# Kernel optimization log

Hardware: AMD Instinct MI355X
Metric: run time of the kernel (lower is better)

Reference implementation:

```python
import jax, jax.numpy as jnp
import numpy as np
from jax import lax

B, N = 16, 4096
S1, S2, K = 512, 256, 32
EPS = 1e-5


def setup_inputs() -> dict:
    key = jax.random.key(0)
    ks = jax.random.split(key, 8)
    p = lambda k, shape: jax.random.normal(k, shape, jnp.float32) * 0.05
    return {
        "x": jax.random.normal(ks[0], (B, 3, N), jnp.float32),
        "w1": p(ks[1], (64, 3)),
        "w2": p(ks[2], (64, 64)),
        "g1": jnp.ones(64, jnp.float32), "b1": jnp.zeros(64, jnp.float32),
        "g2": jnp.ones(64, jnp.float32), "b2": jnp.zeros(64, jnp.float32),
        "sg1_w1": p(ks[3], (128, 128)), "sg1_w2": p(ks[4], (128, 128)),
        "sg1_g1": jnp.ones(128, jnp.float32), "sg1_b1": jnp.zeros(128, jnp.float32),
        "sg1_g2": jnp.ones(128, jnp.float32), "sg1_b2": jnp.zeros(128, jnp.float32),
        "sg2_w1": p(ks[5], (256, 256)), "sg2_w2": p(ks[6], (256, 256)),
        "sg2_g1": jnp.ones(256, jnp.float32), "sg2_b1": jnp.zeros(256, jnp.float32),
        "sg2_g2": jnp.ones(256, jnp.float32), "sg2_b2": jnp.zeros(256, jnp.float32),
    }


def fps(coords, s):
    # furthest point sampling, starts at index 0 (as pointnet2 CUDA kernel)
    Bc, Nc, _ = coords.shape
    def step(carry, _):
        dist, far = carry
        centroid = jnp.take_along_axis(coords, far[:, None, None], axis=1)  # [B,1,3]
        d = jnp.sum((coords - centroid) ** 2, -1)                            # [B,N]
        dist = jnp.minimum(dist, d)
        return (dist, jnp.argmax(dist, -1)), far
    init = (jnp.full((Bc, Nc), 1e10, coords.dtype), jnp.zeros((Bc,), jnp.int32))
    _, idxs = lax.scan(step, init, None, length=s)
    return idxs.T  # [B,s]


def gather(pts, idx):
    # pts [B,N,C], idx [B,...] -> [B,...,C]
    return jax.vmap(lambda p, i: p[i])(pts, idx)


def sqdist(a, b):
    # [B,S,3],[B,N,3] -> [B,S,N]
    return (jnp.sum(a ** 2, -1)[..., None] + jnp.sum(b ** 2, -1)[:, None, :]
            - 2.0 * jnp.einsum('bsc,bnc->bsn', a, b))


def bn_relu_grouped(y, g, b):
    # y [B,s,k,O]; BatchNorm1d over (B*s, O, k) => stats over (0,1,2)
    m = y.mean((0, 1, 2), keepdims=True)
    v = y.var((0, 1, 2), keepdims=True)
    return jax.nn.relu((y - m) / jnp.sqrt(v + EPS) * g + b)


def sg_block(f_bnc, coords, s, w1, g1, b1, w2, g2, b2):
    # f_bnc [B,N,C]; coords [B,N,3]
    fidx = fps(coords, s)                      # [B,s]
    new_xyz = gather(coords, fidx)             # [B,s,3]
    new_feat = gather(f_bnc, fidx)             # [B,s,C]
    d = sqdist(new_xyz, coords)                # [B,s,N]
    _, knn_idx = lax.top_k(-d, K)              # [B,s,K]
    grouped = gather(f_bnc, knn_idx)           # [B,s,K,C]
    center = new_feat[:, :, None]              # [B,s,1,C]
    agg = jnp.concatenate([grouped - center,
                           jnp.broadcast_to(center, grouped.shape)], -1)  # [B,s,K,2C]
    y = bn_relu_grouped(jnp.einsum('bskd,od->bsko', agg, w1), g1, b1)
    y = bn_relu_grouped(jnp.einsum('bskd,od->bsko', y, w2), g2, b2)
    return new_xyz, y.max(2)                   # [B,s,O]


def point_cbr(f, w, g, b):
    # f [B,C,N]; conv1d k=1 + BN (stats over (0,2)) + relu
    y = jnp.einsum('bcn,oc->bon', f, w)
    m = y.mean((0, 2), keepdims=True)
    v = y.var((0, 2), keepdims=True)
    return jax.nn.relu((y - m) / jnp.sqrt(v + EPS) * g[None, :, None] + b[None, :, None])


def reference(x, w1, w2, g1, b1, g2, b2,
              sg1_w1, sg1_w2, sg1_g1, sg1_b1, sg1_g2, sg1_b2,
              sg2_w1, sg2_w2, sg2_g1, sg2_b1, sg2_g2, sg2_b2):
    xyz = x.transpose(0, 2, 1)                                  # [B,N,3]
    f = point_cbr(point_cbr(x, w1, g1, b1), w2, g2, b2)         # [B,64,N]
    xyz1, f1 = sg_block(f.transpose(0, 2, 1), xyz, S1,
                        sg1_w1, sg1_g1, sg1_b1, sg1_w2, sg1_g2, sg1_b2)  # f1 [B,S1,128]
    _, f2 = sg_block(f1, xyz1, S2,
                     sg2_w1, sg2_g1, sg2_b1, sg2_w2, sg2_g2, sg2_b2)     # [B,S2,256]
    return f2.transpose(0, 2, 1)                                # [B,256,S2]
```

## Files before the change

### kernel.cpp

```cpp
#include <hip/hip_runtime.h>

#define EPSF 1e-5f
#define NBINS 16
#define STATS_REGION 8192

using short8  = __attribute__((ext_vector_type(8))) short;
using float4v = __attribute__((ext_vector_type(4))) float;

__device__ __forceinline__ unsigned short f2bf(float f){
    unsigned u = __float_as_uint(f);
    unsigned r = u + 0x7FFFu + ((u >> 16) & 1u);
    return (unsigned short)(r >> 16);
}
__device__ __forceinline__ float bf2f(unsigned short h){
    return __uint_as_float(((unsigned)h) << 16);
}
__device__ __forceinline__ unsigned monou(float f){
    unsigned u = __float_as_uint(f);
    return u ^ (((unsigned)((int)u >> 31)) | 0x80000000u);
}

template<int CTRL, int RMASK>
__device__ __forceinline__ float fmax_dpp(float x){
    int xi = __float_as_int(x);
    int yi = __builtin_amdgcn_update_dpp(xi, xi, CTRL, RMASK, 0xf, false);
    return fmaxf(x, __int_as_float(yi));
}
__device__ __forceinline__ float wave_max_dpp(float x){
    x = fmax_dpp<0x111, 0xf>(x);
    x = fmax_dpp<0x112, 0xf>(x);
    x = fmax_dpp<0x114, 0xf>(x);
    x = fmax_dpp<0x118, 0xf>(x);
    x = fmax_dpp<0x142, 0xa>(x);
    x = fmax_dpp<0x143, 0xc>(x);
    return __int_as_float(__builtin_amdgcn_readlane(__float_as_int(x), 63));
}

__device__ __forceinline__ void compute_ss(const float* __restrict__ st,
                                           const float* __restrict__ g,
                                           const float* __restrict__ bb,
                                           float* lss, int C, float invCnt,
                                           int t, int TPB){
    for (int c = t; c < C; c += TPB){
        float s = 0.f, q = 0.f;
        #pragma unroll 4
        for (int bin = 0; bin < NBINS; bin++){
            s += st[bin * 2 * C + c];
            q += st[bin * 2 * C + C + c];
        }
        float m = s * invCnt;
        float v = q * invCnt - m * m;
        float sc = g[c] / sqrtf(v + EPSF);
        lss[c] = sc;
        lss[C + c] = bb[c] - m * sc;
    }
}

template<int NP, int SO, int AW, bool STRIDED>
__device__ void fps_body(char* smem, const float* __restrict__ coords,
                         int* __restrict__ fidx, float* __restrict__ xyz_out, int b){
    float* lx = (float*)smem;
    float* ly = lx + NP;
    float* lz = ly + NP;
    unsigned long long* red = (unsigned long long*)(lz + NP);
    const int t = threadIdx.x;
    const float* cb = coords + (size_t)b * 3 * NP;
    constexpr int PS = NP / 256;
    #pragma unroll
    for (int i = 0; i < PS; i++){
        int n = i * 256 + t;
        float X, Y, Z;
        if (STRIDED){ X = cb[n]; Y = cb[NP + n]; Z = cb[2*NP + n]; }
        else        { X = cb[n*3]; Y = cb[n*3+1]; Z = cb[n*3+2]; }
        lx[n] = X; ly[n] = Y; lz[n] = Z;
    }
    __syncthreads();
    if (AW == 1 && t >= 64) return;
    constexpr int TPB = AW * 64;
    constexpr int P = NP / TPB;
    float px[P], py[P], pz[P], dist[P];
    #pragma unroll
    for (int i = 0; i < P; i++){
        int n = t * P + i;
        px[i] = lx[n]; py[i] = ly[n]; pz[i] = lz[n];
        dist[i] = 1e10f;
    }
    int cur = 0;
    for (int it = 0; it < SO; ++it){
        if (t == 0){
            fidx[b * SO + it] = cur;
            float* xo = xyz_out + ((size_t)b * SO + it) * 3;
            xo[0] = lx[cur]; xo[1] = ly[cur]; xo[2] = lz[cur];
        }
        float cx = lx[cur], cy = ly[cur], cz = lz[cur];
        float bd = -1.f;
        int bn = 0;
        {
            #pragma clang fp contract(off)
            #pragma unroll
            for (int i = 0; i < P; i++){
                float dx = px[i] - cx, dy = py[i] - cy, dz = pz[i] - cz;
                float d = (dx*dx + dy*dy) + dz*dz;
                float nd = fminf(dist[i], d);
                dist[i] = nd;
                if (nd > bd){ bd = nd; bn = t * P + i; }
            }
        }
        float wm = wave_max_dpp(bd);
        unsigned long long msk = __ballot(bd == wm);
        int wl = (int)(__ffsll(msk) - 1);
        int n_w = __builtin_amdgcn_readlane(bn, wl);
        if constexpr (AW == 1){
            cur = n_w;
        } else {
            int par = it & 1;
            if ((t & 63) == 0){
                red[par * AW + (t >> 6)] = ((unsigned long long)__float_as_uint(wm) << 32)
                                         | (unsigned)(0xFFFFFFFFu - (unsigned)n_w);
            }
            __syncthreads();
            unsigned long long best = red[par * AW];
            #pragma unroll
            for (int j = 1; j < AW; j++){
                unsigned long long v = red[par * AW + j];
                best = best > v ? best : v;
            }
            cur = (int)(0xFFFFFFFFu - (unsigned)(best & 0xFFFFFFFFull));
        }
    }
}

template<int NC, int SO, bool STRIDED>
__device__ void knn_body(const float* __restrict__ coords,
                         const float* __restrict__ samp,
                         int* __restrict__ knno, int row){
    const int b = row / SO, s = row % SO;
    const int lane = threadIdx.x & 63;
    const float* cb = coords + (size_t)b * 3 * NC;
    const float* a = samp + ((size_t)b * SO + s) * 3;
    float ax = a[0], ay = a[1], az = a[2];
    float asq = ax*ax + ay*ay + az*az;
    constexpr int J = NC / 64;
    unsigned long long t8[8];
    #pragma unroll
    for (int i = 0; i < 8; i++) t8[i] = ~0ULL;
    for (int j = 0; j < J; j++){
        int n = j * 64 + lane;
        float bx, by, bz;
        if (STRIDED){ bx = cb[n]; by = cb[NC + n]; bz = cb[2*NC + n]; }
        else        { bx = cb[n*3]; by = cb[n*3+1]; bz = cb[n*3+2]; }
        float bsq = bx*bx + by*by + bz*bz;
        float dot = ax*bx + ay*by + az*bz;
        float d = (asq + bsq) - 2.0f * dot;
        unsigned long long key = ((unsigned long long)monou(d) << 32) | (unsigned)n;
        if (key < t8[7]){
            t8[7] = key;
            #pragma unroll
            for (int i = 6; i >= 0; i--){
                if (t8[i] > t8[i+1]){ unsigned long long tm = t8[i]; t8[i] = t8[i+1]; t8[i+1] = tm; }
            }
        }
    }
    unsigned long long cur = t8[0];
    int myout = 0;
    bool bad = false;
    int popped = 0;
    for (int r = 0; r < 32; r++){
        unsigned long long m = cur;
        #pragma unroll
        for (int o2 = 32; o2 > 0; o2 >>= 1){
            unsigned long long v = __shfl_xor(m, o2, 64);
            m = m < v ? m : v;
        }
        if (lane == r) myout = (int)(unsigned)(m & 0xFFFFFFFFull);
        if (cur == m){
            #pragma unroll
            for (int i = 0; i < 7; i++) t8[i] = t8[i+1];
            t8[7] = ~0ULL;
            cur = t8[0];
            popped++;
            if (J > 8 && popped == 8 && r < 31) bad = true;
        }
    }
    if (__any(bad)){
        unsigned long long last = 0;
        for (int r = 0; r < 32; r++){
            unsigned long long mk = ~0ULL;
            for (int j = 0; j < J; j++){
                int n = j * 64 + lane;
                float bx, by, bz;
                if (STRIDED){ bx = cb[n]; by = cb[NC + n]; bz = cb[2*NC + n]; }
                else        { bx = cb[n*3]; by = cb[n*3+1]; bz = cb[n*3+2]; }
                float bsq = bx*bx + by*by + bz*bz;
                float dot = ax*bx + ay*by + az*bz;
                float d = (asq + bsq) - 2.0f * dot;
                unsigned long long key = ((unsigned long long)monou(d) << 32) | (unsigned)n;
                if (key > last && key < mk) mk = key;
            }
            unsigned long long m = mk;
            #pragma unroll
            for (int o2 = 32; o2 > 0; o2 >>= 1){
                unsigned long long v = __shfl_xor(m, o2, 64);
                m = m < v ? m : v;
            }
            if (lane == r) myout = (int)(unsigned)(m & 0xFFFFFFFFull);
            last = m;
        }
    }
    if (lane < 32) knno[((size_t)b * SO + s) * 32 + lane] = myout;
}

__device__ void pc_body(char* smem, const float* __restrict__ x,
                        const float* __restrict__ w1, const float* __restrict__ w2,
                        const float* __restrict__ g1, const float* __restrict__ b1,
                        const float* __restrict__ xmom, float* __restrict__ y2t,
                        float* __restrict__ stY2, int blk){
    float* w1s  = (float*)smem;
    float* wt   = w1s + 192;
    float* lss1 = wt + 4096;
    float* hS   = lss1 + 128;
    int t = threadIdx.x;
    if (t < 192) w1s[t] = w1[t];
    for (int i = t; i < 4096; i += 256){ int o = i & 63, c = i >> 6; wt[c*64+o] = w2[o*64+c]; }
    __syncthreads();
    if (t < 64){
        float mu0 = xmom[0] * (1.f/65536.f), mu1 = xmom[1] * (1.f/65536.f), mu2 = xmom[2] * (1.f/65536.f);
        float M00 = xmom[3] * (1.f/65536.f), M01 = xmom[4] * (1.f/65536.f), M02 = xmom[5] * (1.f/65536.f);
        float M11 = xmom[6] * (1.f/65536.f), M12 = xmom[7] * (1.f/65536.f), M22 = xmom[8] * (1.f/65536.f);
        float a = w1s[t*3], b = w1s[t*3+1], c = w1s[t*3+2];
        float mo = a*mu0 + b*mu1 + c*mu2;
        float e2 = a*a*M00 + b*b*M11 + c*c*M22 + 2.f*(a*b*M01 + a*c*M02 + b*c*M12);
        float var = e2 - mo*mo;
        float sc = g1[t] / sqrtf(var + EPSF);
        lss1[t] = sc;
        lss1[64 + t] = b1[t] - mo * sc;
    }
    __syncthreads();
    int p = t & 63, cg = t >> 6;
    int point = blk * 64 + p;
    int b = point >> 12, n = point & 4095;
    const float* xb = x + (size_t)b * 12288;
    float x0 = xb[n], x1 = xb[4096 + n], x2 = xb[8192 + n];
    #pragma unroll
    for (int i = 0; i < 16; i++){
        int c = cg * 16 + i;
        float y1 = x0 * w1s[c*3] + x1 * w1s[c*3+1] + x2 * w1s[c*3+2];
        hS[p * 65 + c] = fmaxf(y1 * lss1[c] + lss1[64 + c], 0.f);
    }
    __syncthreads();
    float4v acc[4];
    #pragma unroll
    for (int i = 0; i < 4; i++) acc[i] = (float4v){0.f,0.f,0.f,0.f};
    for (int c = 0; c < 64; c++){
        float hv = hS[p * 65 + c];
        #pragma unroll
        for (int i = 0; i < 4; i++){
            float4v w4 = *(const float4v*)&wt[c*64 + cg*16 + i*4];
            acc[i] += hv * w4;
        }
    }
    float* dst = y2t + (size_t)point * 64 + cg * 16;
    #pragma unroll
    for (int i = 0; i < 4; i++) *(float4v*)(dst + i*4) = acc[i];
    float s16[16], q16[16];
    #pragma unroll
    for (int i = 0; i < 16; i++){
        float v = acc[i >> 2][i & 3];
        s16[i] = v; q16[i] = v * v;
    }
    #pragma unroll
    for (int i = 0; i < 16; i++){
        #pragma unroll
        for (int o = 32; o > 0; o >>= 1){
            s16[i] += __shfl_xor(s16[i], o, 64);
            q16[i] += __shfl_xor(q16[i], o, 64);
        }
    }
    if (p == 0){
        float* sdst = stY2 + (size_t)(blk & (NBINS - 1)) * 128;
        #pragma unroll
        for (int i = 0; i < 16; i++){
            atomicAdd(&sdst[cg * 16 + i], s16[i]);
            atomicAdd(&sdst[64 + cg * 16 + i], q16[i]);
        }
    }
}


template<int O, int D>
__device__ __forceinline__ void pack_body(const float* __restrict__ w,
                                          unsigned short* __restrict__ pk, int tid){
    constexpr int CH = D / 32;
    constexpr int TOT = (O/16) * CH * 64;
    if (tid >= TOT) return;
    int lane = tid & 63;
    int fc = tid >> 6;
    int ch = fc % CH;
    int ot = fc / CH;
    int o  = ot * 16 + (lane & 15);
    int kb = ch * 32 + (lane >> 4) * 8;
    #pragma unroll
    for (int j = 0; j < 8; j++) pk[(size_t)tid * 8 + j] = f2bf(w[(size_t)o * D + kb + j]);
}

template<int D, int O>
__device__ __forceinline__ void mfma_store_y(const short* A, const short* wp,
                                             unsigned short* Y, float* lsum, float* lsq,
                                             int blk, int t){
    constexpr int RS = D + 8;
    constexpr int CH = D / 32;
    constexpr int OPW = (O / 16) / 4;
    int lane = t & 63, wv = t >> 6;
    int col = lane & 15, quad = lane >> 4;
    for (int oi = 0; oi < OPW; ++oi){
        int ot = wv * OPW + oi;
        for (int mt = 0; mt < 4; ++mt){
            float4v acc = {0.f, 0.f, 0.f, 0.f};
            #pragma unroll
            for (int ch = 0; ch < CH; ++ch){
                short8 a  = *(const short8*)(A + (mt*16 + col) * RS + ch*32 + quad*8);
                short8 bf = *(const short8*)(wp + ((size_t)(ot*CH + ch) * 64 + lane) * 8);
                acc = __builtin_amdgcn_mfma_f32_16x16x32_bf16(a, bf, acc, 0, 0, 0);
            }
            float s4 = 0.f, q4 = 0.f;
            size_t rowbase = (size_t)blk * 64 + mt * 16 + quad * 4;
            #pragma unroll
            for (int r = 0; r < 4; r++){
                float v = acc[r];
                s4 += v; q4 += v * v;
                Y[(rowbase + r) * O + ot * 16 + col] = f2bf(v);
            }
            s4 += __shfl_xor(s4, 16, 64); s4 += __shfl_xor(s4, 32, 64);
            q4 += __shfl_xor(q4, 16, 64); q4 += __shfl_xor(q4, 32, 64);
            if (quad == 0){ lsum[ot*16 + col] += s4; lsq[ot*16 + col] += q4; }
        }
    }
}

template<int D, int O>
__device__ __forceinline__ void mfma_maxmin(const short* A, const short* wp,
                                            float2* mxmn, float* lsum, float* lsq,
                                            int blk, int t){
    constexpr int RS = D + 8;
    constexpr int CH = D / 32;
    constexpr int OPW = (O / 16) / 4;
    int lane = t & 63, wv = t >> 6;
    int col = lane & 15, quad = lane >> 4;
    for (int oi = 0; oi < OPW; ++oi){
        int ot = wv * OPW + oi;
        float mx[2] = {-1e30f, -1e30f}, mn[2] = {1e30f, 1e30f};
        for (int mt = 0; mt < 4; ++mt){
            float4v acc = {0.f, 0.f, 0.f, 0.f};
            #pragma unroll
            for (int ch = 0; ch < CH; ++ch){
                short8 a  = *(const short8*)(A + (mt*16 + col) * RS + ch*32 + quad*8);
                short8 bf = *(const short8*)(wp + ((size_t)(ot*CH + ch) * 64 + lane) * 8);
                acc = __builtin_amdgcn_mfma_f32_16x16x32_bf16(a, bf, acc, 0, 0, 0);
            }
            int g = mt >> 1;
            float s4 = 0.f, q4 = 0.f;
            #pragma unroll
            for (int r = 0; r < 4; r++){
                float v = acc[r];
                s4 += v; q4 += v * v;
                mx[g] = fmaxf(mx[g], v);
                mn[g] = fminf(mn[g], v);
            }
            s4 += __shfl_xor(s4, 16, 64); s4 += __shfl_xor(s4, 32, 64);
            q4 += __shfl_xor(q4, 16, 64); q4 += __shfl_xor(q4, 32, 64);
            if (quad == 0){ lsum[ot*16 + col] += s4; lsq[ot*16 + col] += q4; }
        }
        #pragma unroll
        for (int g = 0; g < 2; g++){
            mx[g] = fmaxf(mx[g], __shfl_xor(mx[g], 16, 64));
            mx[g] = fmaxf(mx[g], __shfl_xor(mx[g], 32, 64));
            mn[g] = fminf(mn[g], __shfl_xor(mn[g], 16, 64));
            mn[g] = fminf(mn[g], __shfl_xor(mn[g], 32, 64));
            if (quad == 0){
                mxmn[((size_t)(blk * 2 + g)) * O + ot * 16 + col] = make_float2(mx[g], mn[g]);
            }
        }
    }
}

template<int DH, int O, int S, int NPTS, int MODE>
__device__ void gemm1_body(char* smem, const void* __restrict__ fsrc,
                           const float* __restrict__ fst, const float* __restrict__ fg,
                           const float* __restrict__ fb, float finv,
                           const int* __restrict__ fidx, const int* __restrict__ knn,
                           const short* __restrict__ wp, unsigned short* __restrict__ Y,
                           float* __restrict__ sums, int blk){
    constexpr int D = 2 * DH;
    constexpr int RS = D + 8;
    short* A    = (short*)smem;
    float* lsum = (float*)(smem + 64*RS*2);
    float* lsq  = lsum + O;
    float* lssf = lsq + O;
    int t = threadIdx.x;
    for (int i = t; i < O; i += 256){ lsum[i] = 0.f; lsq[i] = 0.f; }
    compute_ss(fst, fg, fb, lssf, DH, finv, t, 256);
    __syncthreads();
    for (int g = 0; g < 2; ++g){
        int gid = blk * 2 + g;
        int b = gid / S;
        int cidx = fidx[gid];
        int kk = t >> 3;
        int p  = t & 7;
        int nb = knn[(size_t)gid * 32 + kk];
        constexpr int E = D / 8;
        int d0 = p * E;
        short* row = A + (g * 32 + kk) * RS;
        if (MODE == 1){
            const float* fcp = (const float*)fsrc + ((size_t)b * NPTS + cidx) * DH;
            const float* fnp = (const float*)fsrc + ((size_t)b * NPTS + nb) * DH;
            #pragma unroll
            for (int e = 0; e < E; e++){
                int d = d0 + e;
                float v;
                if (d < DH){
                    float a = fmaxf(fnp[d] * lssf[d] + lssf[DH + d], 0.f);
                    float c = fmaxf(fcp[d] * lssf[d] + lssf[DH + d], 0.f);
                    v = a - c;
                } else {
                    v = fmaxf(fcp[d - DH] * lssf[d - DH] + lssf[DH + d - DH], 0.f);
                }
                row[d] = (short)f2bf(v);
            }
        } else {
            const float2* fcp = (const float2*)fsrc + ((size_t)b * NPTS + cidx) * DH;
            const float2* fnp = (const float2*)fsrc + ((size_t)b * NPTS + nb) * DH;
            #pragma unroll
            for (int e = 0; e < E; e++){
                int d = d0 + e;
                float v;
                if (d < DH){
                    float sc = lssf[d], sh = lssf[DH + d];
                    float2 a2 = fnp[d], c2 = fcp[d];
                    float av = fmaxf((sc > 0.f ? a2.x : a2.y) * sc + sh, 0.f);
                    float cv = fmaxf((sc > 0.f ? c2.x : c2.y) * sc + sh, 0.f);
                    v = av - cv;
                } else {
                    int dd = d - DH;
                    float sc = lssf[dd], sh = lssf[DH + dd];
                    float2 c2 = fcp[dd];
                    v = fmaxf((sc > 0.f ? c2.x : c2.y) * sc + sh, 0.f);
                }
                row[d] = (short)f2bf(v);
            }
        }
    }
    __syncthreads();
    mfma_store_y<D, O>(A, wp, Y, lsum, lsq, blk, t);
    __syncthreads();
    float* dst = sums + (size_t)(blk & (NBINS - 1)) * 2 * O;
    for (int i = t; i < O; i += 256){
        atomicAdd(&dst[i], lsum[i]);
        atomicAdd(&dst[O + i], lsq[i]);
    }
}

template<int D, int O>
__device__ void gemm2m_body(char* smem, const unsigned short* __restrict__ Yin,
                            const float* __restrict__ st, const float* __restrict__ g,
                            const float* __restrict__ bb, float inv,
                            const short* __restrict__ wp, float2* __restrict__ mxmn,
                            float* __restrict__ sums, int blk){
    constexpr int RS = D + 8;
    short* A    = (short*)smem;
    float* lsum = (float*)(smem + 64*RS*2);
    float* lsq  = lsum + O;
    float* lss  = lsq + O;
    int t = threadIdx.x;
    for (int i = t; i < O; i += 256){ lsum[i] = 0.f; lsq[i] = 0.f; }
    compute_ss(st, g, bb, lss, D, inv, t, 256);
    __syncthreads();
    {
        int row = t >> 2;
        int d0 = (t & 3) * (D / 4);
        const unsigned short* src = Yin + ((size_t)blk * 64 + row) * D + d0;
        short* dst = A + row * RS + d0;
        #pragma unroll
        for (int e = 0; e < D/4; e++){
            float v = bf2f(src[e]);
            int d = d0 + e;
            v = fmaxf(v * lss[d] + lss[D + d], 0.f);
            dst[e] = (short)f2bf(v);
        }
    }
    __syncthreads();
    mfma_maxmin<D, O>(A, wp, mxmn, lsum, lsq, blk, t);
    __syncthreads();
    float* dst = sums + (size_t)(blk & (NBINS - 1)) * 2 * O;
    for (int i = t; i < O; i += 256){
        atomicAdd(&dst[i], lsum[i]);
        atomicAdd(&dst[O + i], lsq[i]);
    }
}


__global__ __launch_bounds__(256) void k1_statsx_pack(const float* __restrict__ x,
                                                      float* __restrict__ xmom,
                                                      const float* w1, const float* w2,
                                                      const float* w3, const float* w4,
                                                      unsigned short* p1, unsigned short* p2,
                                                      unsigned short* p3, unsigned short* p4){
    int blk = blockIdx.x, t = threadIdx.x;
    if (blk == 0){
        float a[9] = {0,0,0,0,0,0,0,0,0};
        for (int gid = t; gid < 65536; gid += 256){
            int b = gid >> 12, n = gid & 4095;
            const float* xb = x + (size_t)b * 12288;
            float x0 = xb[n], x1 = xb[4096 + n], x2 = xb[8192 + n];
            a[0] += x0; a[1] += x1; a[2] += x2;
            a[3] += x0*x0; a[4] += x0*x1; a[5] += x0*x2;
            a[6] += x1*x1; a[7] += x1*x2; a[8] += x2*x2;
        }
        __shared__ float red[4][9];
        #pragma unroll
        for (int k = 0; k < 9; k++){
            float v = a[k];
            for (int o = 32; o > 0; o >>= 1) v += __shfl_down(v, o, 64);
            a[k] = v;
        }
        if ((t & 63) == 0){
            #pragma unroll
            for (int k = 0; k < 9; k++) red[t >> 6][k] = a[k];
        }
        __syncthreads();
        if (t == 0){
            #pragma unroll
            for (int k = 0; k < 9; k++)
                xmom[k] = red[0][k] + red[1][k] + red[2][k] + red[3][k];
        }
    } else {
        int pb = blk - 1;
        if (pb < 8)       pack_body<128,128>(w1, p1, pb * 256 + t);
        else if (pb < 16) pack_body<128,128>(w2, p2, (pb - 8) * 256 + t);
        else if (pb < 48) pack_body<256,256>(w3, p3, (pb - 16) * 256 + t);
        else              pack_body<256,256>(w4, p4, (pb - 48) * 256 + t);
    }
}

__global__ __launch_bounds__(256) void k2_fps1_pc(const float* __restrict__ x,
                                                  int* __restrict__ fidx1, float* __restrict__ xyz1,
                                                  const float* w1, const float* w2,
                                                  const float* g1, const float* b1,
                                                  const float* __restrict__ xmom,
                                                  float* __restrict__ y2t,
                                                  float* __restrict__ stY2){
    extern __shared__ char smem[];
    if (blockIdx.x < 16) fps_body<4096,512,4,true>(smem, x, fidx1, xyz1, blockIdx.x);
    else                 pc_body(smem, x, w1, w2, g1, b1, xmom, y2t, stY2, blockIdx.x - 16);
}

__global__ __launch_bounds__(256) void k3_knn1(const float* __restrict__ x,
                                               const float* __restrict__ xyz1,
                                               int* __restrict__ knn1){
    int row = blockIdx.x * 4 + (threadIdx.x >> 6);
    knn_body<4096,512,true>(x, xyz1, knn1, row);
}

__global__ __launch_bounds__(256) void k4_fps2_gemm1a(const float* __restrict__ xyz1,
                                                      int* __restrict__ fidx2, float* __restrict__ xyz2,
                                                      const float* __restrict__ y2t,
                                                      const float* __restrict__ stY2,
                                                      const float* g2, const float* b2,
                                                      const int* __restrict__ fidx1,
                                                      const int* __restrict__ knn1,
                                                      const short* __restrict__ wp1,
                                                      unsigned short* __restrict__ Y1,
                                                      float* __restrict__ stG1a){
    extern __shared__ char smem[];
    if (blockIdx.x < 16)
        fps_body<512,256,1,false>(smem, xyz1, fidx2, xyz2, blockIdx.x);
    else
        gemm1_body<64,128,512,4096,1>(smem, y2t, stY2, g2, b2, 1.f/65536.f,
                                      fidx1, knn1, wp1, Y1, stG1a, blockIdx.x - 16);
}

__global__ __launch_bounds__(256) void k5_knn2_gemm2ma(const float* __restrict__ xyz1,
                                                       const float* __restrict__ xyz2,
                                                       int* __restrict__ knn2,
                                                       const unsigned short* __restrict__ Y1,
                                                       const float* __restrict__ stG1a,
                                                       const float* s1g1, const float* s1b1,
                                                       const short* __restrict__ wp2,
                                                       float2* __restrict__ mxmn1,
                                                       float* __restrict__ stG2a){
    extern __shared__ char smem[];
    if (blockIdx.x < 1024){
        int row = blockIdx.x * 4 + (threadIdx.x >> 6);
        knn_body<512,256,false>(xyz1, xyz2, knn2, row);
    } else {
        gemm2m_body<128,128>(smem, Y1, stG1a, s1g1, s1b1, 1.f/262144.f,
                             wp2, mxmn1, stG2a, blockIdx.x - 1024);
    }
}

template<int DH, int O, int S, int NPTS, int MODE>
__global__ __launch_bounds__(256) void gemm1_kernel(const void* fsrc, const float* fst,
                                                    const float* fg, const float* fb, float finv,
                                                    const int* fidx, const int* knn,
                                                    const short* wp, unsigned short* Y,
                                                    float* sums){
    extern __shared__ char smem[];
    gemm1_body<DH,O,S,NPTS,MODE>(smem, fsrc, fst, fg, fb, finv, fidx, knn, wp, Y, sums, blockIdx.x);
}

template<int D, int O>
__global__ __launch_bounds__(256) void gemm2m_kernel(const unsigned short* Yin, const float* st,
                                                     const float* g, const float* bb, float inv,
                                                     const short* wp, float2* mxmn, float* sums){
    extern __shared__ char smem[];
    gemm2m_body<D,O>(smem, Yin, st, g, bb, inv, wp, mxmn, sums, blockIdx.x);
}

__global__ __launch_bounds__(256) void final_out_kernel(const float2* __restrict__ mxmn,
                                                        const float* __restrict__ st,
                                                        const float* __restrict__ g,
                                                        const float* __restrict__ bb,
                                                        float inv,
                                                        float* __restrict__ out){
    __shared__ float lss[512];
    __shared__ float tile[64][65];
    int t = threadIdx.x;
    compute_ss(st, g, bb, lss, 256, inv, t, 256);
    __syncthreads();
    int blk = blockIdx.x;
    int b = blk >> 4;
    int ot = (blk >> 2) & 3, stt = blk & 3;
    int o_in = t & 63, sg = t >> 6;
    int o = ot * 64 + o_in;
    float sc = lss[o], sh = lss[256 + o];
    for (int si = 0; si < 16; si++){
        int s = stt * 64 + sg * 16 + si;
        int row = b * 256 + s;
        float2 v2 = mxmn[(size_t)row * 256 + o];
        float v = (sc > 0.f ? v2.x : v2.y) * sc + sh;
        tile[sg * 16 + si][o_in] = fmaxf(v, 0.f);
    }
    __syncthreads();
    int s_in = t & 63, og = t >> 6;
    for (int oj = 0; oj < 16; oj++){
        int oo = ot * 64 + og * 16 + oj;
        out[(size_t)b * 65536 + (size_t)oo * 256 + stt * 64 + s_in] = tile[s_in][og * 16 + oj];
    }
}

extern "C" void kernel_launch(void* const* d_in, const int* in_sizes, int n_in,
                              void* d_out, int out_size, void* d_ws, size_t ws_size,
                              hipStream_t stream) {
    const float* x    = (const float*)d_in[0];
    const float* w1   = (const float*)d_in[1];
    const float* w2   = (const float*)d_in[2];
    const float* g1   = (const float*)d_in[3];
    const float* b1   = (const float*)d_in[4];
    const float* g2   = (const float*)d_in[5];
    const float* b2   = (const float*)d_in[6];
    const float* s1w1 = (const float*)d_in[7];
    const float* s1w2 = (const float*)d_in[8];
    const float* s1g1 = (const float*)d_in[9];
    const float* s1b1 = (const float*)d_in[10];
    const float* s1g2 = (const float*)d_in[11];
    const float* s1b2 = (const float*)d_in[12];
    const float* s2w1 = (const float*)d_in[13];
    const float* s2w2 = (const float*)d_in[14];
    const float* s2g1 = (const float*)d_in[15];
    const float* s2b1 = (const float*)d_in[16];
    const float* s2g2 = (const float*)d_in[17];
    const float* s2b2 = (const float*)d_in[18];
    float* out = (float*)d_out;

    char* ws = (char*)d_ws;
    size_t off = 0;
    auto take = [&](size_t bytes){ size_t r = off; off += (bytes + 255) & ~(size_t)255; return r; };
    float* y2t     = (float*)(ws + take(16u*4096u*64u*4u));
    float2* mxmn1  = (float2*)(ws + take(8192u*128u*8u));
    float2* mxmn2  = (float2*)(ws + take(4096u*256u*8u));
    int*   fidx1   = (int*)  (ws + take(16u*512u*4u));
    float* xyz1    = (float*)(ws + take(16u*512u*3u*4u));
    int*   fidx2   = (int*)  (ws + take(16u*256u*4u));
    float* xyz2    = (float*)(ws + take(16u*256u*3u*4u));
    int*   knn1    = (int*)  (ws + take(16u*512u*32u*4u));
    int*   knn2    = (int*)  (ws + take(16u*256u*32u*4u));
    unsigned short* wp1 = (unsigned short*)(ws + take(128u*128u*2u));
    unsigned short* wp2 = (unsigned short*)(ws + take(128u*128u*2u));
    unsigned short* wp3 = (unsigned short*)(ws + take(256u*256u*2u));
    unsigned short* wp4 = (unsigned short*)(ws + take(256u*256u*2u));
    float* stats   = (float*)(ws + take(6u*STATS_REGION*4u));
    char*  regA    = ws + take(67108864u);
    (void)in_sizes; (void)n_in; (void)out_size; (void)ws_size;

    float* xmom    = stats + 0*STATS_REGION;
    float* stY2    = stats + 1*STATS_REGION;
    float* stG1a   = stats + 2*STATS_REGION;
    float* stG2a   = stats + 3*STATS_REGION;
    float* stG1b   = stats + 4*STATS_REGION;
    float* stG2b   = stats + 5*STATS_REGION;

    unsigned short* Y1 = (unsigned short*)regA;

    hipMemsetAsync(stats, 0, 6u*STATS_REGION*4u, stream);

    k1_statsx_pack<<<81, 256, 0, stream>>>(x, xmom, s1w1, s1w2, s2w1, s2w2, wp1, wp2, wp3, wp4);
    k2_fps1_pc<<<1040, 256, 49216, stream>>>(x, fidx1, xyz1, w1, w2, g1, b1, xmom, y2t, stY2);
    k3_knn1<<<2048, 256, 0, stream>>>(x, xyz1, knn1);
    k4_fps2_gemm1a<<<4112, 256, 18944, stream>>>(xyz1, fidx2, xyz2, y2t, stY2, g2, b2,
                                                 fidx1, knn1, (const short*)wp1, Y1, stG1a);
    k5_knn2_gemm2ma<<<5120, 256, 19456, stream>>>(xyz1, xyz2, knn2, Y1, stG1a, s1g1, s1b1,
                                                  (const short*)wp2, mxmn1, stG2a);
    gemm1_kernel<128,256,256,512,2><<<2048, 256, 36864, stream>>>(
        mxmn1, stG2a, s1g2, s1b2, 1.f/262144.f, fidx2, knn2, (const short*)wp3, Y1, stG1b);
    gemm2m_kernel<256,256><<<2048, 256, 37888, stream>>>(
        Y1, stG1b, s2g1, s2b1, 1.f/131072.f, (const short*)wp4, mxmn2, stG2b);
    final_out_kernel<<<256, 256, 0, stream>>>(mxmn2, stG2b, s2g2, s2b2, 1.f/131072.f, out);
}
```

Measured before the change: 939.9 us.

## Vectorize LDS row stores, raise FPS priority, parallelize input moment stats

Measured after the change: 884.8 us. 5.9% less time.

```diff
diff --git a/kernel.cpp b/kernel.cpp
--- a/kernel.cpp
+++ b/kernel.cpp
@@ -59,6 +59,7 @@
 template<int NP, int SO, int AW, bool STRIDED>
 __device__ void fps_body(char* smem, const float* __restrict__ coords,
                          int* __restrict__ fidx, float* __restrict__ xyz_out, int b){
+    asm volatile("s_setprio 3");
     float* lx = (float*)smem;
     float* ly = lx + NP;
     float* lz = ly + NP;
@@ -414,38 +415,48 @@
             const float* fcp = (const float*)fsrc + ((size_t)b * NPTS + cidx) * DH;
             const float* fnp = (const float*)fsrc + ((size_t)b * NPTS + nb) * DH;
             #pragma unroll
-            for (int e = 0; e < E; e++){
-                int d = d0 + e;
-                float v;
-                if (d < DH){
-                    float a = fmaxf(fnp[d] * lssf[d] + lssf[DH + d], 0.f);
-                    float c = fmaxf(fcp[d] * lssf[d] + lssf[DH + d], 0.f);
-                    v = a - c;
-                } else {
-                    v = fmaxf(fcp[d - DH] * lssf[d - DH] + lssf[DH + d - DH], 0.f);
+            for (int e8 = 0; e8 < E; e8 += 8){
+                short8 pk;
+                #pragma unroll
+                for (int e = 0; e < 8; e++){
+                    int d = d0 + e8 + e;
+                    float v;
+                    if (d < DH){
+                        float a = fmaxf(fnp[d] * lssf[d] + lssf[DH + d], 0.f);
+                        float c = fmaxf(fcp[d] * lssf[d] + lssf[DH + d], 0.f);
+                        v = a - c;
+                    } else {
+                        v = fmaxf(fcp[d - DH] * lssf[d - DH] + lssf[DH + d - DH], 0.f);
+                    }
+                    pk[e] = (short)f2bf(v);
                 }
-                row[d] = (short)f2bf(v);
+                *(short8*)(row + d0 + e8) = pk;
             }
         } else {
             const float2* fcp = (const float2*)fsrc + ((size_t)b * NPTS + cidx) * DH;
             const float2* fnp = (const float2*)fsrc + ((size_t)b * NPTS + nb) * DH;
             #pragma unroll
-            for (int e = 0; e < E; e++){
-                int d = d0 + e;
-                float v;
-                if (d < DH){
-                    float sc = lssf[d], sh = lssf[DH + d];
-                    float2 a2 = fnp[d], c2 = fcp[d];
-                    float av = fmaxf((sc > 0.f ? a2.x : a2.y) * sc + sh, 0.f);
-                    float cv = fmaxf((sc > 0.f ? c2.x : c2.y) * sc + sh, 0.f);
-                    v = av - cv;
-                } else {
-                    int dd = d - DH;
-                    float sc = lssf[dd], sh = lssf[DH + dd];
-                    float2 c2 = fcp[dd];
-                    v = fmaxf((sc > 0.f ? c2.x : c2.y) * sc + sh, 0.f);
+            for (int e8 = 0; e8 < E; e8 += 8){
+                short8 pk;
+                #pragma unroll
+                for (int e = 0; e < 8; e++){
+                    int d = d0 + e8 + e;
+                    float v;
+                    if (d < DH){
+                        float sc = lssf[d], sh = lssf[DH + d];
+                        float2 a2 = fnp[d], c2 = fcp[d];
+                        float av = fmaxf((sc > 0.f ? a2.x : a2.y) * sc + sh, 0.f);
+                        float cv = fmaxf((sc > 0.f ? c2.x : c2.y) * sc + sh, 0.f);
+                        v = av - cv;
+                    } else {
+                        int dd = d - DH;
+                        float sc = lssf[dd], sh = lssf[DH + dd];
+                        float2 c2 = fcp[dd];
+                        v = fmaxf((sc > 0.f ? c2.x : c2.y) * sc + sh, 0.f);
+                    }
+                    pk[e] = (short)f2bf(v);
                 }
-                row[d] = (short)f2bf(v);
+                *(short8*)(row + d0 + e8) = pk;
             }
         }
     }
@@ -480,11 +491,16 @@
         const unsigned short* src = Yin + ((size_t)blk * 64 + row) * D + d0;
         short* dst = A + row * RS + d0;
         #pragma unroll
-        for (int e = 0; e < D/4; e++){
-            float v = bf2f(src[e]);
-            int d = d0 + e;
-            v = fmaxf(v * lss[d] + lss[D + d], 0.f);
-            dst[e] = (short)f2bf(v);
+        for (int e8 = 0; e8 < D/4; e8 += 8){
+            short8 pk;
+            #pragma unroll
+            for (int e = 0; e < 8; e++){
+                float v = bf2f(src[e8 + e]);
+                int d = d0 + e8 + e;
+                v = fmaxf(v * lss[d] + lss[D + d], 0.f);
+                pk[e] = (short)f2bf(v);
+            }
+            *(short8*)(dst + e8) = pk;
         }
     }
     __syncthreads();
@@ -505,9 +521,10 @@
                                                       unsigned short* p1, unsigned short* p2,
                                                       unsigned short* p3, unsigned short* p4){
     int blk = blockIdx.x, t = threadIdx.x;
-    if (blk == 0){
+    if (blk < 16){
         float a[9] = {0,0,0,0,0,0,0,0,0};
-        for (int gid = t; gid < 65536; gid += 256){
+        for (int i = 0; i < 16; i++){
+            int gid = blk * 4096 + i * 256 + t;
             int b = gid >> 12, n = gid & 4095;
             const float* xb = x + (size_t)b * 12288;
             float x0 = xb[n], x1 = xb[4096 + n], x2 = xb[8192 + n];
@@ -530,10 +547,10 @@
         if (t == 0){
             #pragma unroll
             for (int k = 0; k < 9; k++)
-                xmom[k] = red[0][k] + red[1][k] + red[2][k] + red[3][k];
+                atomicAdd(&xmom[k], red[0][k] + red[1][k] + red[2][k] + red[3][k]);
         }
     } else {
-        int pb = blk - 1;
+        int pb = blk - 16;
         if (pb < 8)       pack_body<128,128>(w1, p1, pb * 256 + t);
         else if (pb < 16) pack_body<128,128>(w2, p2, (pb - 8) * 256 + t);
         else if (pb < 48) pack_body<256,256>(w3, p3, (pb - 16) * 256 + t);
@@ -702,7 +719,7 @@
 
     hipMemsetAsync(stats, 0, 6u*STATS_REGION*4u, stream);
 
-    k1_statsx_pack<<<81, 256, 0, stream>>>(x, xmom, s1w1, s1w2, s2w1, s2w2, wp1, wp2, wp3, wp4);
+    k1_statsx_pack<<<96, 256, 0, stream>>>(x, xmom, s1w1, s1w2, s2w1, s2w2, wp1, wp2, wp3, wp4);
     k2_fps1_pc<<<1040, 256, 49216, stream>>>(x, fidx1, xyz1, w1, w2, g1, b1, xmom, y2t, stY2);
     k3_knn1<<<2048, 256, 0, stream>>>(x, xyz1, knn1);
     k4_fps2_gemm1a<<<4112, 256, 18944, stream>>>(xyz1, fidx2, xyz2, y2t, stY2, g2, b2,
```
